# Kernel optimization log

Hardware: AMD Instinct MI355X
Metric: run time of the kernel (lower is better)

The kernel has to match this reference:

```python
import jax, jax.numpy as jnp
import numpy as np

ENC_H = 512
DEC_H = 512
FIELD = 128

def setup_inputs() -> dict:
    key = jax.random.key(0)
    ks = jax.random.split(key, 12)
    B, S, T = 8, 256, 32
    def lin(k, fan_in, fan_out):
        k1, k2 = jax.random.split(k)
        bound = 1.0 / np.sqrt(fan_in)
        W = jax.random.uniform(k1, (fan_in, fan_out), minval=-bound, maxval=bound, dtype=jnp.float32)
        b = jax.random.uniform(k2, (fan_out,), minval=-bound, maxval=bound, dtype=jnp.float32)
        return W, b
    W1, b1 = lin(ks[0], ENC_H, DEC_H)
    W2, b2 = lin(ks[1], DEC_H, DEC_H)
    W3, b3 = lin(ks[2], FIELD, DEC_H)
    W4, b4 = lin(ks[3], DEC_H, DEC_H)
    return {
        "output": jax.random.normal(ks[4], (B, T, DEC_H), dtype=jnp.float32),
        "encoder_hidden": jax.random.normal(ks[5], (S, B, ENC_H), dtype=jnp.float32),
        "input_z": jax.random.normal(ks[6], (B, S, FIELD), dtype=jnp.float32),
        "W1": W1, "b1": b1, "W2": W2, "b2": b2,
        "W3": W3, "b3": b3, "W4": W4, "b4": b4,
    }

def reference(output, encoder_hidden, input_z, W1, b1, W2, b2, W3, b3, W4, b4):
    S, B, He = encoder_hidden.shape
    # tanh(lin1(encoder_hidden)) then .view(B, S, D)  (reshape, NOT transpose -- faithful to torch .view)
    out_hs = jnp.tanh(encoder_hidden @ W1 + b1).reshape(B, S, -1)      # [B,S,D]
    enc_h = encoder_hidden.reshape(B, S, He)                            # [B,S,He]
    out_fds = jnp.tanh(input_z @ W3 + b3)                               # [B,S,D]
    out2 = jnp.tanh(output @ W2 + b2)                                   # [B,T,D]
    out3 = jnp.tanh(output @ W4 + b4)                                   # [B,T,D]
    # vectorized over timesteps: g1[b,s,t,d] = out_hs[b,s,d]*out2[b,t,d]
    g1 = out_hs[:, :, None, :] * out2[:, None, :, :]                    # [B,S,T,D]
    alpha = jax.nn.softmax(g1, axis=1)                                  # softmax over S, per feature d
    g2 = out_fds[:, :, None, :] * out3[:, None, :, :]                   # [B,S,T,D]
    beta = jax.nn.softmax(g2, axis=1)
    q = alpha * beta                                                    # [B,S,T,D]
    qn = jax.lax.stop_gradient(jnp.sum(q, axis=1, keepdims=True))       # detached normalizer
    gamma = q / qn                                                      # [B,S,T,D]
    contex = jnp.sum(gamma * enc_h[:, :, None, :], axis=1)              # [B,T,D]
    concat_vectors = jnp.concatenate([output, contex], axis=-1)         # [B,T,2D]
    # attn: list over t of gamma[:, :, t, :] -> stacked [B,T,S,D]
    attn = jnp.transpose(gamma, (0, 2, 1, 3))
    return (concat_vectors, attn)
```

## Files before the change

kernel.cpp:

```cpp
#include <hip/hip_runtime.h>


typedef __attribute__((ext_vector_type(8))) short bf16x8;
typedef __attribute__((ext_vector_type(4))) float f32x4;

__device__ __forceinline__ unsigned short f2bf(float x) {
    union { float f; unsigned u; } v; v.f = x;
    unsigned r = v.u + 0x7fffu + ((v.u >> 16) & 1u);
    return (unsigned short)(r >> 16);
}

__global__ __launch_bounds__(256) void prep_k(
    const float* __restrict__ E, const float* __restrict__ Z, const float* __restrict__ O,
    const float* __restrict__ W1, const float* __restrict__ W2,
    const float* __restrict__ W3, const float* __restrict__ W4,
    unsigned short* __restrict__ Ebf, unsigned short* __restrict__ Zbf,
    unsigned short* __restrict__ Obf,
    unsigned short* __restrict__ W1T, unsigned short* __restrict__ W2T,
    unsigned short* __restrict__ W3T, unsigned short* __restrict__ W4T)
{
    int bid = blockIdx.x;
    if (bid < 1408) {
        const float* src; unsigned short* dst; int base;
        if (bid < 1024)      { src = E; dst = Ebf; base = bid; }
        else if (bid < 1280) { src = Z; dst = Zbf; base = bid - 1024; }
        else                 { src = O; dst = Obf; base = bid - 1280; }
        int i = base * 1024 + threadIdx.x * 4;
        float4 v = *(const float4*)(src + i);
        ushort4 r;
        r.x = f2bf(v.x); r.y = f2bf(v.y); r.z = f2bf(v.z); r.w = f2bf(v.w);
        *(ushort4*)(dst + i) = r;
        return;
    }
    int tb = bid - 1408;
    const float* W; unsigned short* WT; int K;
    if (tb < 256)      {            W = W1; WT = W1T; K = 512; }
    else if (tb < 512) { tb -= 256; W = W2; WT = W2T; K = 512; }
    else if (tb < 576) { tb -= 512; W = W3; WT = W3T; K = 128; }
    else               { tb -= 576; W = W4; WT = W4T; K = 512; }
    int n0 = (tb & 15) * 32;
    int k0 = (tb >> 4) * 32;
    __shared__ float tile[32][33];
    int tx = threadIdx.x & 31, ty = threadIdx.x >> 5;
    #pragma unroll
    for (int i = 0; i < 32; i += 8)
        tile[ty + i][tx] = W[(k0 + ty + i) * 512 + n0 + tx];
    __syncthreads();
    #pragma unroll
    for (int i = 0; i < 32; i += 8)
        WT[(n0 + ty + i) * K + k0 + tx] = f2bf(tile[tx][ty + i]);
}

__global__ __launch_bounds__(256) void gemm_all_k(
    const unsigned short* __restrict__ Ebf, const unsigned short* __restrict__ Zbf,
    const unsigned short* __restrict__ Obf,
    const unsigned short* __restrict__ W1T, const unsigned short* __restrict__ W3T,
    const unsigned short* __restrict__ W2T, const unsigned short* __restrict__ W4T,
    const float* __restrict__ b1, const float* __restrict__ b3,
    const float* __restrict__ b2, const float* __restrict__ b4,
    float* __restrict__ L1, float* __restrict__ F,
    float* __restrict__ O2, float* __restrict__ O3)
{
    int id = blockIdx.x;
    const unsigned short* A; const unsigned short* BT; const float* bias; float* C;
    int K;
    if (id < 256)      {             A = Ebf; BT = W1T; bias = b1; C = L1; K = 512; }
    else if (id < 512) { id -= 256;  A = Zbf; BT = W3T; bias = b3; C = F;  K = 128; }
    else if (id < 544) { id -= 512;  A = Obf; BT = W2T; bias = b2; C = O2; K = 512; }
    else               { id -= 544;  A = Obf; BT = W4T; bias = b4; C = O3; K = 512; }
    int m0 = (id >> 3) * 64;
    int n0 = (id & 7) * 64;

    __shared__ unsigned short As[64 * 72];
    __shared__ unsigned short Bs[64 * 72];

    int tid  = threadIdx.x;
    int wave = tid >> 6;
    int lane = tid & 63;
    int lm   = lane & 15;
    int lq   = lane >> 4;

    int srow = tid >> 2;
    int scol = (tid & 3) * 16;

    f32x4 acc[4];
    #pragma unroll
    for (int c = 0; c < 4; ++c) acc[c] = f32x4{0.f, 0.f, 0.f, 0.f};

    for (int k0 = 0; k0 < K; k0 += 64) {
        __syncthreads();
        const unsigned short* Ap = &A[(m0 + srow) * K + k0 + scol];
        const unsigned short* Bp = &BT[(n0 + srow) * K + k0 + scol];
        *(uint4*)(&As[srow * 72 + scol])     = *(const uint4*)(Ap);
        *(uint4*)(&As[srow * 72 + scol + 8]) = *(const uint4*)(Ap + 8);
        *(uint4*)(&Bs[srow * 72 + scol])     = *(const uint4*)(Bp);
        *(uint4*)(&Bs[srow * 72 + scol + 8]) = *(const uint4*)(Bp + 8);
        __syncthreads();
        #pragma unroll
        for (int ks = 0; ks < 2; ++ks) {
            bf16x8 af = *(const bf16x8*)(&As[(wave * 16 + lm) * 72 + ks * 32 + lq * 8]);
            #pragma unroll
            for (int c = 0; c < 4; ++c) {
                bf16x8 bfr = *(const bf16x8*)(&Bs[(c * 16 + lm) * 72 + ks * 32 + lq * 8]);
                acc[c] = __builtin_amdgcn_mfma_f32_16x16x32_bf16(af, bfr, acc[c], 0, 0, 0);
            }
        }
    }

    #pragma unroll
    for (int c = 0; c < 4; ++c) {
        int col = n0 + c * 16 + lm;
        float bv = bias[col];
        #pragma unroll
        for (int r = 0; r < 4; ++r) {
            int row = m0 + wave * 16 + lq * 4 + r;
            float x = acc[c][r] + bv;
            x = fminf(fmaxf(x, -15.f), 15.f);
            float t = __expf(2.0f * x);
            C[row * 512 + col] = (t - 1.0f) / (t + 1.0f);
        }
    }
}

__global__ __launch_bounds__(256) void attn_partial_k(
    const float* __restrict__ L1, const float* __restrict__ F,
    const float* __restrict__ O2, const float* __restrict__ O3,
    const float* __restrict__ Enc,
    float* __restrict__ sum_p, float* __restrict__ csum_p)
{
    int b  = blockIdx.x >> 4;
    int sc = blockIdx.x & 15;
    int tc = blockIdx.y;
    int d  = blockIdx.z * 256 + threadIdx.x;

    float c2[8], c3[8], sum[8], csum[8];
    #pragma unroll
    for (int i = 0; i < 8; ++i) {
        int bt = b * 32 + tc * 8 + i;
        c2[i] = O2[bt * 512 + d];
        c3[i] = O3[bt * 512 + d];
        sum[i] = 0.f; csum[i] = 0.f;
    }

    int s0 = sc * 16;
    const float* L1b = L1  + (b * 256 + s0) * 512 + d;
    const float* Fb  = F   + (b * 256 + s0) * 512 + d;
    const float* Eb  = Enc + (b * 256 + s0) * 512 + d;

    #pragma unroll 2
    for (int s = 0; s < 16; ++s) {
        float l1 = L1b[s * 512];
        float f  = Fb[s * 512];
        float eh = Eb[s * 512];
        #pragma unroll
        for (int i = 0; i < 8; ++i) {
            float e = __expf(l1 * c2[i] + f * c3[i]);
            sum[i]  += e;
            csum[i] += e * eh;
        }
    }

    #pragma unroll
    for (int i = 0; i < 8; ++i) {
        int idx = ((b * 16 + sc) * 32 + tc * 8 + i) * 512 + d;
        sum_p[idx]  = sum[i];
        csum_p[idx] = csum[i];
    }
}

__global__ __launch_bounds__(256) void attn_finalize_k(
    const float* __restrict__ sum_p, const float* __restrict__ csum_p,
    const float* __restrict__ Out,
    float* __restrict__ out0, float* __restrict__ invA)
{
    int bt = blockIdx.x;
    int d  = blockIdx.y * 256 + threadIdx.x;
    int b  = bt >> 5, t = bt & 31;

    float sum = 0.f, csum = 0.f;
    #pragma unroll
    for (int sc = 0; sc < 16; ++sc) {
        int idx = ((b * 16 + sc) * 32 + t) * 512 + d;
        sum  += sum_p[idx];
        csum += csum_p[idx];
    }
    float inv = 1.0f / sum;
    invA[bt * 512 + d] = inv;
    out0[bt * 1024 + d]       = Out[bt * 512 + d];
    out0[bt * 1024 + 512 + d] = csum * inv;
}

__global__ __launch_bounds__(256) void attn_write_k(
    const float* __restrict__ L1, const float* __restrict__ F,
    const float* __restrict__ O2, const float* __restrict__ O3,
    const float* __restrict__ invA,
    float* __restrict__ attn)
{
    int b     = blockIdx.x;
    int sbase = blockIdx.y * 8 + (threadIdx.x >> 7) * 4;
    int d4    = (threadIdx.x & 127) * 4;

    f32x4 l1[4], f[4];
    #pragma unroll
    for (int j = 0; j < 4; ++j) {
        l1[j] = *(const f32x4*)(L1 + (b * 256 + sbase + j) * 512 + d4);
        f[j]  = *(const f32x4*)(F  + (b * 256 + sbase + j) * 512 + d4);
    }

    for (int t = 0; t < 32; ++t) {
        int bt = b * 32 + t;
        f32x4 c2 = *(const f32x4*)(O2   + bt * 512 + d4);
        f32x4 c3 = *(const f32x4*)(O3   + bt * 512 + d4);
        f32x4 iv = *(const f32x4*)(invA + bt * 512 + d4);
        #pragma unroll
        for (int j = 0; j < 4; ++j) {
            f32x4 g;
            g[0] = __expf(l1[j][0] * c2[0] + f[j][0] * c3[0]) * iv[0];
            g[1] = __expf(l1[j][1] * c2[1] + f[j][1] * c3[1]) * iv[1];
            g[2] = __expf(l1[j][2] * c2[2] + f[j][2] * c3[2]) * iv[2];
            g[3] = __expf(l1[j][3] * c2[3] + f[j][3] * c3[3]) * iv[3];
            __builtin_nontemporal_store(
                g, (f32x4*)(attn + ((size_t)(bt * 256 + sbase + j)) * 512 + d4));
        }
    }
}

extern "C" void kernel_launch(void* const* d_in, const int* in_sizes, int n_in,
                              void* d_out, int out_size, void* d_ws, size_t ws_size,
                              hipStream_t stream)
{
    const float* Out = (const float*)d_in[0];
    const float* Enc = (const float*)d_in[1];
    const float* Z   = (const float*)d_in[2];
    const float* W1  = (const float*)d_in[3];
    const float* b1  = (const float*)d_in[4];
    const float* W2  = (const float*)d_in[5];
    const float* b2  = (const float*)d_in[6];
    const float* W3  = (const float*)d_in[7];
    const float* b3  = (const float*)d_in[8];
    const float* W4  = (const float*)d_in[9];
    const float* b4  = (const float*)d_in[10];

    char* ws = (char*)d_ws;
    size_t off = 0;
    auto alloc = [&](size_t n) -> char* {
        char* p = ws + off; off += (n + 255) & ~(size_t)255; return p;
    };
    unsigned short* Ebf = (unsigned short*)alloc(1048576 * 2);
    unsigned short* Zbf = (unsigned short*)alloc(262144 * 2);
    unsigned short* Obf = (unsigned short*)alloc(131072 * 2);
    unsigned short* W1T = (unsigned short*)alloc(262144 * 2);
    unsigned short* W2T = (unsigned short*)alloc(262144 * 2);
    unsigned short* W3T = (unsigned short*)alloc(65536 * 2);
    unsigned short* W4T = (unsigned short*)alloc(262144 * 2);
    float* L1    = (float*)alloc(1048576 * 4);
    float* F     = (float*)alloc(1048576 * 4);
    float* O2    = (float*)alloc(131072 * 4);
    float* O3    = (float*)alloc(131072 * 4);
    float* sum_p = (float*)alloc(2097152 * 4);
    float* csum_p= (float*)alloc(2097152 * 4);
    float* invA  = (float*)alloc(131072 * 4);

    float* out0 = (float*)d_out;
    float* attn = out0 + 262144;

    hipLaunchKernelGGL(prep_k, dim3(2240), dim3(256), 0, stream,
                       Enc, Z, Out, W1, W2, W3, W4,
                       Ebf, Zbf, Obf, W1T, W2T, W3T, W4T);
    hipLaunchKernelGGL(gemm_all_k, dim3(576), dim3(256), 0, stream,
                       Ebf, Zbf, Obf, W1T, W3T, W2T, W4T,
                       b1, b3, b2, b4, L1, F, O2, O3);
    hipLaunchKernelGGL(attn_partial_k, dim3(128, 4, 2), dim3(256), 0, stream,
                       L1, F, O2, O3, Enc, sum_p, csum_p);
    hipLaunchKernelGGL(attn_finalize_k, dim3(256, 2), dim3(256), 0, stream,
                       sum_p, csum_p, Out, out0, invA);
    hipLaunchKernelGGL(attn_write_k, dim3(8, 32), dim3(256), 0, stream,
                       L1, F, O2, O3, invA, attn);
}
```

Before: 202.3 us.

## Replace partial-sum buffers with atomics, fold finalize into write kernel, split T

The partial kernel now accumulates its per-chunk sums straight into small [B,T,D] buffers with atomicAdd, and prep_k zeroes those buffers first. This removes the 16x-sized partial buffers and the separate finalize kernel. The write kernel computes the reciprocal itself and writes the concatenated output, and its grid gains a T dimension (8x more blocks, 4 timesteps each) for more parallelism. The cost is atomic contention and non-deterministic summation order, and each split block reloads its L1/F tile.

```diff
diff --git a/kernel.cpp b/kernel.cpp
--- a/kernel.cpp
+++ b/kernel.cpp
@@ -17,9 +17,16 @@
     unsigned short* __restrict__ Ebf, unsigned short* __restrict__ Zbf,
     unsigned short* __restrict__ Obf,
     unsigned short* __restrict__ W1T, unsigned short* __restrict__ W2T,
-    unsigned short* __restrict__ W3T, unsigned short* __restrict__ W4T)
+    unsigned short* __restrict__ W3T, unsigned short* __restrict__ W4T,
+    float* __restrict__ sum, float* __restrict__ csum)
 {
     int bid = blockIdx.x;
+    if (bid >= 2240) {
+        int idx = (bid - 2240) * 1024 + threadIdx.x * 4;
+        float* p = (idx < 131072) ? (sum + idx) : (csum + (idx - 131072));
+        *(f32x4*)p = f32x4{0.f, 0.f, 0.f, 0.f};
+        return;
+    }
     if (bid < 1408) {
         const float* src; unsigned short* dst; int base;
         if (bid < 1024)      { src = E; dst = Ebf; base = bid; }
@@ -126,20 +133,20 @@
     const float* __restrict__ L1, const float* __restrict__ F,
     const float* __restrict__ O2, const float* __restrict__ O3,
     const float* __restrict__ Enc,
-    float* __restrict__ sum_p, float* __restrict__ csum_p)
+    float* __restrict__ sum, float* __restrict__ csum)
 {
     int b  = blockIdx.x >> 4;
     int sc = blockIdx.x & 15;
     int tc = blockIdx.y;
     int d  = blockIdx.z * 256 + threadIdx.x;
 
-    float c2[8], c3[8], sum[8], csum[8];
+    float c2[8], c3[8], s_[8], cs[8];
     #pragma unroll
     for (int i = 0; i < 8; ++i) {
         int bt = b * 32 + tc * 8 + i;
         c2[i] = O2[bt * 512 + d];
         c3[i] = O3[bt * 512 + d];
-        sum[i] = 0.f; csum[i] = 0.f;
+        s_[i] = 0.f; cs[i] = 0.f;
     }
 
     int s0 = sc * 16;
@@ -155,49 +162,29 @@
         #pragma unroll
         for (int i = 0; i < 8; ++i) {
             float e = __expf(l1 * c2[i] + f * c3[i]);
-            sum[i]  += e;
-            csum[i] += e * eh;
+            s_[i]  += e;
+            cs[i]  += e * eh;
         }
     }
 
     #pragma unroll
     for (int i = 0; i < 8; ++i) {
-        int idx = ((b * 16 + sc) * 32 + tc * 8 + i) * 512 + d;
-        sum_p[idx]  = sum[i];
-        csum_p[idx] = csum[i];
-    }
-}
-
-__global__ __launch_bounds__(256) void attn_finalize_k(
-    const float* __restrict__ sum_p, const float* __restrict__ csum_p,
-    const float* __restrict__ Out,
-    float* __restrict__ out0, float* __restrict__ invA)
-{
-    int bt = blockIdx.x;
-    int d  = blockIdx.y * 256 + threadIdx.x;
-    int b  = bt >> 5, t = bt & 31;
-
-    float sum = 0.f, csum = 0.f;
-    #pragma unroll
-    for (int sc = 0; sc < 16; ++sc) {
-        int idx = ((b * 16 + sc) * 32 + t) * 512 + d;
-        sum  += sum_p[idx];
-        csum += csum_p[idx];
-    }
-    float inv = 1.0f / sum;
-    invA[bt * 512 + d] = inv;
-    out0[bt * 1024 + d]       = Out[bt * 512 + d];
-    out0[bt * 1024 + 512 + d] = csum * inv;
+        int idx = (b * 32 + tc * 8 + i) * 512 + d;
+        atomicAdd(&sum[idx],  s_[i]);
+        atomicAdd(&csum[idx], cs[i]);
+    }
 }
 
 __global__ __launch_bounds__(256) void attn_write_k(
     const float* __restrict__ L1, const float* __restrict__ F,
     const float* __restrict__ O2, const float* __restrict__ O3,
-    const float* __restrict__ invA,
-    float* __restrict__ attn)
+    const float* __restrict__ sum, const float* __restrict__ csum,
+    const float* __restrict__ Out,
+    float* __restrict__ out0, float* __restrict__ attn)
 {
     int b     = blockIdx.x;
     int sbase = blockIdx.y * 8 + (threadIdx.x >> 7) * 4;
+    int tz    = blockIdx.z;
     int d4    = (threadIdx.x & 127) * 4;
 
     f32x4 l1[4], f[4];
@@ -207,11 +194,14 @@
         f[j]  = *(const f32x4*)(F  + (b * 256 + sbase + j) * 512 + d4);
     }
 
-    for (int t = 0; t < 32; ++t) {
-        int bt = b * 32 + t;
-        f32x4 c2 = *(const f32x4*)(O2   + bt * 512 + d4);
-        f32x4 c3 = *(const f32x4*)(O3   + bt * 512 + d4);
-        f32x4 iv = *(const f32x4*)(invA + bt * 512 + d4);
+    for (int ti = 0; ti < 4; ++ti) {
+        int bt = b * 32 + tz * 4 + ti;
+        f32x4 c2 = *(const f32x4*)(O2  + bt * 512 + d4);
+        f32x4 c3 = *(const f32x4*)(O3  + bt * 512 + d4);
+        f32x4 sm = *(const f32x4*)(sum + bt * 512 + d4);
+        f32x4 iv;
+        iv[0] = 1.0f / sm[0]; iv[1] = 1.0f / sm[1];
+        iv[2] = 1.0f / sm[2]; iv[3] = 1.0f / sm[3];
         #pragma unroll
         for (int j = 0; j < 4; ++j) {
             f32x4 g;
@@ -221,6 +211,15 @@
             g[3] = __expf(l1[j][3] * c2[3] + f[j][3] * c3[3]) * iv[3];
             __builtin_nontemporal_store(
                 g, (f32x4*)(attn + ((size_t)(bt * 256 + sbase + j)) * 512 + d4));
+        }
+        if (blockIdx.y == 0 && threadIdx.x < 128) {
+            f32x4 ov = *(const f32x4*)(Out  + bt * 512 + d4);
+            f32x4 cv = *(const f32x4*)(csum + bt * 512 + d4);
+            f32x4 cx;
+            cx[0] = cv[0] * iv[0]; cx[1] = cv[1] * iv[1];
+            cx[2] = cv[2] * iv[2]; cx[3] = cv[3] * iv[3];
+            *(f32x4*)(out0 + bt * 1024 + d4)       = ov;
+            *(f32x4*)(out0 + bt * 1024 + 512 + d4) = cx;
         }
     }
 }
@@ -253,27 +252,24 @@
     unsigned short* W2T = (unsigned short*)alloc(262144 * 2);
     unsigned short* W3T = (unsigned short*)alloc(65536 * 2);
     unsigned short* W4T = (unsigned short*)alloc(262144 * 2);
-    float* L1    = (float*)alloc(1048576 * 4);
-    float* F     = (float*)alloc(1048576 * 4);
-    float* O2    = (float*)alloc(131072 * 4);
-    float* O3    = (float*)alloc(131072 * 4);
-    float* sum_p = (float*)alloc(2097152 * 4);
-    float* csum_p= (float*)alloc(2097152 * 4);
-    float* invA  = (float*)alloc(131072 * 4);
+    float* L1   = (float*)alloc(1048576 * 4);
+    float* F    = (float*)alloc(1048576 * 4);
+    float* O2   = (float*)alloc(131072 * 4);
+    float* O3   = (float*)alloc(131072 * 4);
+    float* sum  = (float*)alloc(131072 * 4);
+    float* csum = (float*)alloc(131072 * 4);
 
     float* out0 = (float*)d_out;
     float* attn = out0 + 262144;
 
-    hipLaunchKernelGGL(prep_k, dim3(2240), dim3(256), 0, stream,
+    hipLaunchKernelGGL(prep_k, dim3(2496), dim3(256), 0, stream,
                        Enc, Z, Out, W1, W2, W3, W4,
-                       Ebf, Zbf, Obf, W1T, W2T, W3T, W4T);
+                       Ebf, Zbf, Obf, W1T, W2T, W3T, W4T, sum, csum);
     hipLaunchKernelGGL(gemm_all_k, dim3(576), dim3(256), 0, stream,
                        Ebf, Zbf, Obf, W1T, W3T, W2T, W4T,
                        b1, b3, b2, b4, L1, F, O2, O3);
     hipLaunchKernelGGL(attn_partial_k, dim3(128, 4, 2), dim3(256), 0, stream,
-                       L1, F, O2, O3, Enc, sum_p, csum_p);
-    hipLaunchKernelGGL(attn_finalize_k, dim3(256, 2), dim3(256), 0, stream,
-                       sum_p, csum_p, Out, out0, invA);
-    hipLaunchKernelGGL(attn_write_k, dim3(8, 32), dim3(256), 0, stream,
-                       L1, F, O2, O3, invA, attn);
-}
+                       L1, F, O2, O3, Enc, sum, csum);
+    hipLaunchKernelGGL(attn_write_k, dim3(8, 32, 8), dim3(256), 0, stream,
+                       L1, F, O2, O3, sum, csum, Out, out0, attn);
+}
```

Measured after the change: 209.7 us. 3.6% more time.

## Fuse attention partial, finalize and write kernels into one per-(b,t,d-chunk) kernel

Applied to the files above, without the earlier changes.

Replaces the three-kernel attention pipeline (partial sums over S chunks, finalize, and recompute-and-write) with a single kernel. Each block handles one (b,t) and a 64-wide d slice, computes all 256 exponentials once and keeps them in registers, reduces sum and csum through LDS, then scales and writes attn directly. This removes the partial-sum workspace traffic, two launches and the second exp pass. In exchange, L1, F and Enc are re-read for every t (32 times) instead of being reused across t, and register pressure rises from holding 16 float4 values per thread.

```diff
diff --git a/kernel.cpp b/kernel.cpp
--- a/kernel.cpp
+++ b/kernel.cpp
@@ -122,106 +122,82 @@
     }
 }
 
-__global__ __launch_bounds__(256) void attn_partial_k(
+__global__ __launch_bounds__(256, 4) void attn_fused_k(
     const float* __restrict__ L1, const float* __restrict__ F,
     const float* __restrict__ O2, const float* __restrict__ O3,
-    const float* __restrict__ Enc,
-    float* __restrict__ sum_p, float* __restrict__ csum_p)
-{
-    int b  = blockIdx.x >> 4;
-    int sc = blockIdx.x & 15;
-    int tc = blockIdx.y;
-    int d  = blockIdx.z * 256 + threadIdx.x;
-
-    float c2[8], c3[8], sum[8], csum[8];
-    #pragma unroll
-    for (int i = 0; i < 8; ++i) {
-        int bt = b * 32 + tc * 8 + i;
-        c2[i] = O2[bt * 512 + d];
-        c3[i] = O3[bt * 512 + d];
-        sum[i] = 0.f; csum[i] = 0.f;
-    }
-
-    int s0 = sc * 16;
-    const float* L1b = L1  + (b * 256 + s0) * 512 + d;
-    const float* Fb  = F   + (b * 256 + s0) * 512 + d;
-    const float* Eb  = Enc + (b * 256 + s0) * 512 + d;
-
-    #pragma unroll 2
-    for (int s = 0; s < 16; ++s) {
-        float l1 = L1b[s * 512];
-        float f  = Fb[s * 512];
-        float eh = Eb[s * 512];
+    const float* __restrict__ Enc, const float* __restrict__ Out,
+    float* __restrict__ out0, float* __restrict__ attn)
+{
+    int b  = blockIdx.x;
+    int dc = blockIdx.y;
+    int t  = blockIdx.z;
+    int bt = b * 32 + t;
+    int dl = (threadIdx.x & 15) * 4;
+    int sr = threadIdx.x >> 4;
+    int d0 = dc * 64;
+
+    __shared__ float red_s[16 * 64];
+    __shared__ float red_c[16 * 64];
+    __shared__ float iv_lds[64];
+
+    const float* L1b = L1  + (b * 256) * 512 + d0 + dl;
+    const float* Fb  = F   + (b * 256) * 512 + d0 + dl;
+    const float* Eb  = Enc + (b * 256) * 512 + d0 + dl;
+
+    f32x4 c2 = *(const f32x4*)(O2 + bt * 512 + d0 + dl);
+    f32x4 c3 = *(const f32x4*)(O3 + bt * 512 + d0 + dl);
+
+    f32x4 e[16];
+    f32x4 sum = f32x4{0.f, 0.f, 0.f, 0.f};
+    f32x4 csum = f32x4{0.f, 0.f, 0.f, 0.f};
+
+    #pragma unroll
+    for (int i = 0; i < 16; ++i) {
+        int s = i * 16 + sr;
+        f32x4 l1 = *(const f32x4*)(L1b + s * 512);
+        f32x4 f  = *(const f32x4*)(Fb  + s * 512);
+        f32x4 eh = *(const f32x4*)(Eb  + s * 512);
+        f32x4 ev;
+        ev[0] = __expf(l1[0] * c2[0] + f[0] * c3[0]);
+        ev[1] = __expf(l1[1] * c2[1] + f[1] * c3[1]);
+        ev[2] = __expf(l1[2] * c2[2] + f[2] * c3[2]);
+        ev[3] = __expf(l1[3] * c2[3] + f[3] * c3[3]);
+        e[i] = ev;
+        sum[0] += ev[0]; sum[1] += ev[1]; sum[2] += ev[2]; sum[3] += ev[3];
+        csum[0] += ev[0] * eh[0]; csum[1] += ev[1] * eh[1];
+        csum[2] += ev[2] * eh[2]; csum[3] += ev[3] * eh[3];
+    }
+
+    *(f32x4*)(&red_s[sr * 64 + dl]) = sum;
+    *(f32x4*)(&red_c[sr * 64 + dl]) = csum;
+    __syncthreads();
+
+    if (threadIdx.x < 64) {
+        int d = threadIdx.x;
+        float s_ = 0.f, c_ = 0.f;
         #pragma unroll
-        for (int i = 0; i < 8; ++i) {
-            float e = __expf(l1 * c2[i] + f * c3[i]);
-            sum[i]  += e;
-            csum[i] += e * eh;
+        for (int r = 0; r < 16; ++r) {
+            s_ += red_s[r * 64 + d];
+            c_ += red_c[r * 64 + d];
         }
-    }
-
-    #pragma unroll
-    for (int i = 0; i < 8; ++i) {
-        int idx = ((b * 16 + sc) * 32 + tc * 8 + i) * 512 + d;
-        sum_p[idx]  = sum[i];
-        csum_p[idx] = csum[i];
-    }
-}
-
-__global__ __launch_bounds__(256) void attn_finalize_k(
-    const float* __restrict__ sum_p, const float* __restrict__ csum_p,
-    const float* __restrict__ Out,
-    float* __restrict__ out0, float* __restrict__ invA)
-{
-    int bt = blockIdx.x;
-    int d  = blockIdx.y * 256 + threadIdx.x;
-    int b  = bt >> 5, t = bt & 31;
-
-    float sum = 0.f, csum = 0.f;
-    #pragma unroll
-    for (int sc = 0; sc < 16; ++sc) {
-        int idx = ((b * 16 + sc) * 32 + t) * 512 + d;
-        sum  += sum_p[idx];
-        csum += csum_p[idx];
-    }
-    float inv = 1.0f / sum;
-    invA[bt * 512 + d] = inv;
-    out0[bt * 1024 + d]       = Out[bt * 512 + d];
-    out0[bt * 1024 + 512 + d] = csum * inv;
-}
-
-__global__ __launch_bounds__(256) void attn_write_k(
-    const float* __restrict__ L1, const float* __restrict__ F,
-    const float* __restrict__ O2, const float* __restrict__ O3,
-    const float* __restrict__ invA,
-    float* __restrict__ attn)
-{
-    int b     = blockIdx.x;
-    int sbase = blockIdx.y * 8 + (threadIdx.x >> 7) * 4;
-    int d4    = (threadIdx.x & 127) * 4;
-
-    f32x4 l1[4], f[4];
-    #pragma unroll
-    for (int j = 0; j < 4; ++j) {
-        l1[j] = *(const f32x4*)(L1 + (b * 256 + sbase + j) * 512 + d4);
-        f[j]  = *(const f32x4*)(F  + (b * 256 + sbase + j) * 512 + d4);
-    }
-
-    for (int t = 0; t < 32; ++t) {
-        int bt = b * 32 + t;
-        f32x4 c2 = *(const f32x4*)(O2   + bt * 512 + d4);
-        f32x4 c3 = *(const f32x4*)(O3   + bt * 512 + d4);
-        f32x4 iv = *(const f32x4*)(invA + bt * 512 + d4);
-        #pragma unroll
-        for (int j = 0; j < 4; ++j) {
-            f32x4 g;
-            g[0] = __expf(l1[j][0] * c2[0] + f[j][0] * c3[0]) * iv[0];
-            g[1] = __expf(l1[j][1] * c2[1] + f[j][1] * c3[1]) * iv[1];
-            g[2] = __expf(l1[j][2] * c2[2] + f[j][2] * c3[2]) * iv[2];
-            g[3] = __expf(l1[j][3] * c2[3] + f[j][3] * c3[3]) * iv[3];
-            __builtin_nontemporal_store(
-                g, (f32x4*)(attn + ((size_t)(bt * 256 + sbase + j)) * 512 + d4));
-        }
+        float inv = 1.0f / s_;
+        iv_lds[d] = inv;
+        out0[bt * 1024 + 512 + d0 + d] = c_ * inv;
+        out0[bt * 1024 + d0 + d]       = Out[bt * 512 + d0 + d];
+    }
+    __syncthreads();
+
+    f32x4 iv = *(const f32x4*)(&iv_lds[dl]);
+    float* ab = attn + ((size_t)bt * 256) * 512 + d0 + dl;
+    #pragma unroll
+    for (int i = 0; i < 16; ++i) {
+        int s = i * 16 + sr;
+        f32x4 g;
+        g[0] = e[i][0] * iv[0];
+        g[1] = e[i][1] * iv[1];
+        g[2] = e[i][2] * iv[2];
+        g[3] = e[i][3] * iv[3];
+        __builtin_nontemporal_store(g, (f32x4*)(ab + (size_t)s * 512));
     }
 }
 
@@ -253,13 +229,10 @@
     unsigned short* W2T = (unsigned short*)alloc(262144 * 2);
     unsigned short* W3T = (unsigned short*)alloc(65536 * 2);
     unsigned short* W4T = (unsigned short*)alloc(262144 * 2);
-    float* L1    = (float*)alloc(1048576 * 4);
-    float* F     = (float*)alloc(1048576 * 4);
-    float* O2    = (float*)alloc(131072 * 4);
-    float* O3    = (float*)alloc(131072 * 4);
-    float* sum_p = (float*)alloc(2097152 * 4);
-    float* csum_p= (float*)alloc(2097152 * 4);
-    float* invA  = (float*)alloc(131072 * 4);
+    float* L1 = (float*)alloc(1048576 * 4);
+    float* F  = (float*)alloc(1048576 * 4);
+    float* O2 = (float*)alloc(131072 * 4);
+    float* O3 = (float*)alloc(131072 * 4);
 
     float* out0 = (float*)d_out;
     float* attn = out0 + 262144;
@@ -270,10 +243,6 @@
     hipLaunchKernelGGL(gemm_all_k, dim3(576), dim3(256), 0, stream,
                        Ebf, Zbf, Obf, W1T, W3T, W2T, W4T,
                        b1, b3, b2, b4, L1, F, O2, O3);
-    hipLaunchKernelGGL(attn_partial_k, dim3(128, 4, 2), dim3(256), 0, stream,
-                       L1, F, O2, O3, Enc, sum_p, csum_p);
-    hipLaunchKernelGGL(attn_finalize_k, dim3(256, 2), dim3(256), 0, stream,
-                       sum_p, csum_p, Out, out0, invA);
-    hipLaunchKernelGGL(attn_write_k, dim3(8, 32), dim3(256), 0, stream,
-                       L1, F, O2, O3, invA, attn);
-}
+    hipLaunchKernelGGL(attn_fused_k, dim3(8, 8, 32), dim3(256), 0, stream,
+                       L1, F, O2, O3, Enc, Out, out0, attn);
+}
```

Result: no change. 201.9 us (-0.2%).
